# Performance work log

Hardware: AMD Instinct MI355X
Metric: run time of the kernel (lower is better)

The kernel has to match this reference:

```python
import jax, jax.numpy as jnp
import numpy as np

NUM_HEADS = 8
C = 512


def setup_inputs() -> dict:
    key = jax.random.key(0)
    ks = jax.random.split(key, 8)
    B, D, H, W = 1, 16, 16, 16
    x = jax.random.normal(ks[0], (B, C, D, H, W), dtype=jnp.float32)
    s = 1.0 / np.sqrt(C)
    Wq = jax.random.normal(ks[1], (C, C), dtype=jnp.float32) * s
    Wk = jax.random.normal(ks[2], (C, C), dtype=jnp.float32) * s
    Wv = jax.random.normal(ks[3], (C, C), dtype=jnp.float32) * s
    bq = jax.random.normal(ks[4], (C,), dtype=jnp.float32) * 0.01
    bk = jax.random.normal(ks[5], (C,), dtype=jnp.float32) * 0.01
    bv = jax.random.normal(ks[6], (C,), dtype=jnp.float32) * 0.01
    # torch inits gamma to 0; use 0.5 so the attention branch contributes
    gamma = jnp.full((1,), 0.5, dtype=jnp.float32)
    return {"x": x, "Wq": Wq, "bq": bq, "Wk": Wk, "bk": bk, "Wv": Wv, "bv": bv, "gamma": gamma}


def _attn(x, Wq, bq, Wk, bk, Wv, bv, gamma):
    B, Cc, D, H, W = x.shape
    nh = NUM_HEADS
    hd = Cc // nh
    N = D * H * W

    def proj(Wm, bm):
        # 1x1x1 Conv3d == channel GEMM
        y = jnp.einsum('oc,bcdhw->bodhw', Wm, x) + bm[None, :, None, None, None]
        y = y.reshape(B, nh, hd, D, H, W)            # [B, nh, hd, D, H, W]
        y = jnp.moveaxis(y, 2, -1)                    # [B, nh, D, H, W, hd]
        return y.reshape(B * nh, N, hd)               # [B*nh, N, hd]

    q = proj(Wq, bq)
    k = proj(Wk, bk)
    v = proj(Wv, bv)

    # NOTE: original module has NO 1/sqrt(head_dim) scaling -- faithful.
    energy = jnp.einsum('bnd,bmd->bnm', q, k)         # [B*nh, N, N]
    attention = jax.nn.softmax(energy, axis=-1)
    out = jnp.einsum('bnm,bmd->bnd', attention, v)    # [B*nh, N, hd]

    # Faithful (buggy-in-original) reshape: [B, N, nh, hd] row-major into [B, C, D, H, W]
    out = out.reshape(B, nh, N, hd).transpose(0, 2, 1, 3).reshape(B, Cc, D, H, W)
    return gamma[0] * out + x


def reference(x, Wq, bq, Wk, bk, Wv, bv, gamma):
    return _attn(x, Wq, bq, Wk, bk, Wv, bv, gamma)
```

## Files before the change

kernel.cpp:

```cpp
#include <hip/hip_runtime.h>

typedef unsigned short u16;
typedef __attribute__((ext_vector_type(4))) float f32x4;
typedef __attribute__((ext_vector_type(8))) short s16x8;
typedef __attribute__((ext_vector_type(4))) unsigned short u16x4;
typedef __attribute__((ext_vector_type(8))) unsigned short u16x8;
typedef __attribute__((ext_vector_type(2))) unsigned int u32x2;

#define MFMA(a, b, c) __builtin_amdgcn_mfma_f32_16x16x32_bf16((a), (b), (c), 0, 0, 0)

#define XT_HI 0u
#define XT_LO 2097152u
#define W_HI  4194304u
#define W_LO  4980736u
#define Q_HI  5767168u
#define Q_LO  7864320u
#define K_HI  9961472u
#define K_LO  12058624u
#define V_HI  14155776u
#define V_LO  16252928u
#define WS_BYTES_U16 36700160u

__device__ __forceinline__ u16 f2bf(float f) {
  union { float f; unsigned u; } v; v.f = f;
  unsigned r = v.u + 0x7fffu + ((v.u >> 16) & 1u);
  return (u16)(r >> 16);
}
__device__ __forceinline__ float bf2f(u16 h) {
  union { unsigned u; float f; } v; v.u = ((unsigned)h) << 16;
  return v.f;
}
__device__ __forceinline__ unsigned pk2(float a, float b) {
  return (unsigned)f2bf(a) | ((unsigned)f2bf(b) << 16);
}
__device__ __forceinline__ void gload16(const void* g, void* l) {
  __builtin_amdgcn_global_load_lds(
      (const __attribute__((address_space(1))) void*)g,
      (__attribute__((address_space(3))) void*)l, 16, 0, 0);
}

__global__ __launch_bounds__(256) void prep_w(const float* __restrict__ wq,
                                              const float* __restrict__ wk,
                                              const float* __restrict__ wv,
                                              u16* __restrict__ ws) {
  unsigned t = blockIdx.x * 256u + threadIdx.x;
  unsigned idx = t * 4u;
  unsigned which = idx >> 18;
  unsigned rem = idx & 262143u;
  const float* src = (which == 0) ? wq : (which == 1) ? wk : wv;
  f32x4 v = *(const f32x4*)(src + rem);
  u16x4 h, l;
#pragma unroll
  for (int i = 0; i < 4; ++i) {
    u16 hb = f2bf(v[i]);
    h[i] = hb;
    l[i] = f2bf(v[i] - bf2f(hb));
  }
  *(u16x4*)(ws + W_HI + idx) = h;
  *(u16x4*)(ws + W_LO + idx) = l;
}

__global__ __launch_bounds__(256) void prep_xt(const float* __restrict__ x,
                                               u16* __restrict__ ws) {
  __shared__ float tile[64][65];
  unsigned t = threadIdx.x;
  unsigned n0 = blockIdx.x * 64u, c0 = blockIdx.y * 64u;
  unsigned cl = t >> 2, ns = (t & 3u) * 16u;
  const float* src = x + (c0 + cl) * 4096u + n0 + ns;
#pragma unroll
  for (int j = 0; j < 16; j += 4) {
    f32x4 v = *(const f32x4*)(src + j);
#pragma unroll
    for (int e = 0; e < 4; ++e) tile[cl][ns + j + e] = v[e];
  }
  __syncthreads();
  unsigned nl = t >> 2, cs = (t & 3u) * 16u;
  u16x8 vh0, vh1, vl0, vl1;
#pragma unroll
  for (int j = 0; j < 16; ++j) {
    float v = tile[cs + j][nl];
    u16 hb = f2bf(v);
    u16 lb = f2bf(v - bf2f(hb));
    if (j < 8) { vh0[j] = hb; vl0[j] = lb; }
    else       { vh1[j - 8] = hb; vl1[j - 8] = lb; }
  }
  unsigned off = (n0 + nl) * 512u + c0 + cs;
  *(u16x8*)(ws + XT_HI + off) = vh0;
  *(u16x8*)(ws + XT_HI + off + 8u) = vh1;
  *(u16x8*)(ws + XT_LO + off) = vl0;
  *(u16x8*)(ws + XT_LO + off + 8u) = vl1;
}

__global__ __launch_bounds__(256) void proj(const float* __restrict__ bq,
                                            const float* __restrict__ bk,
                                            const float* __restrict__ bv,
                                            u16* __restrict__ ws) {
  __shared__ u16 sm[24576];
  const unsigned t = threadIdx.x, w = t >> 6, lane = t & 63u;
  const unsigned g4 = lane >> 4, c = lane & 15u;
  const unsigned z = blockIdx.z;
  const unsigned m0 = blockIdx.y * 64u, n0 = blockIdx.x * 128u;
  const unsigned wo = w >> 1, wn = w & 1u;

  const u16* WHp = ws + W_HI + z * 262144u;
  const u16* WLp = ws + W_LO + z * 262144u;
  const u16* XH = ws + XT_HI;
  const u16* XL = ws + XT_LO;

  f32x4 acc[2][4];
#pragma unroll
  for (int a = 0; a < 2; ++a)
#pragma unroll
    for (int b = 0; b < 4; ++b) acc[a][b] = (f32x4){0.f, 0.f, 0.f, 0.f};

  const unsigned r_l = lane >> 3;
  const unsigned cl_ = lane & 7u;

  for (unsigned it = 0; it < 8; ++it) {
    unsigned k0 = it * 64u;
#pragma unroll
    for (unsigned j = 0; j < 12; ++j) {
      unsigned s = w * 12u + j;
      if (s < 8u) {
        unsigned r = 8u * s + r_l; unsigned cg = cl_ ^ (r & 7u);
        gload16(WHp + (m0 + r) * 512u + k0 + 8u * cg, sm + s * 512u);
      } else if (s < 16u) {
        unsigned sl = s - 8u; unsigned r = 8u * sl + r_l; unsigned cg = cl_ ^ (r & 7u);
        gload16(WLp + (m0 + r) * 512u + k0 + 8u * cg, sm + 4096u + sl * 512u);
      } else if (s < 32u) {
        unsigned sl = s - 16u; unsigned r = 8u * sl + r_l; unsigned cg = cl_ ^ (r & 7u);
        gload16(XH + (n0 + r) * 512u + k0 + 8u * cg, sm + 8192u + sl * 512u);
      } else {
        unsigned sl = s - 32u; unsigned r = 8u * sl + r_l; unsigned cg = cl_ ^ (r & 7u);
        gload16(XL + (n0 + r) * 512u + k0 + 8u * cg, sm + 16384u + sl * 512u);
      }
    }
    __syncthreads();

    s16x8 ah[2][2], al[2][2];
#pragma unroll
    for (int mr = 0; mr < 2; ++mr)
#pragma unroll
      for (int ks = 0; ks < 2; ++ks) {
        unsigned row = 32u * wo + 16u * mr + c;
        unsigned idx = row * 64u + (((g4 + 4u * ks) ^ (row & 7u)) * 8u);
        ah[mr][ks] = *(const s16x8*)(sm + idx);
        al[mr][ks] = *(const s16x8*)(sm + 4096u + idx);
      }
#pragma unroll
    for (int ks = 0; ks < 2; ++ks)
#pragma unroll
      for (int nr = 0; nr < 4; ++nr) {
        unsigned row = 64u * wn + 16u * nr + c;
        unsigned idx = row * 64u + (((g4 + 4u * ks) ^ (row & 7u)) * 8u);
        s16x8 bh = *(const s16x8*)(sm + 8192u + idx);
        s16x8 bl = *(const s16x8*)(sm + 16384u + idx);
#pragma unroll
        for (int mr = 0; mr < 2; ++mr) {
          acc[mr][nr] = MFMA(ah[mr][ks], bh, acc[mr][nr]);
          acc[mr][nr] = MFMA(ah[mr][ks], bl, acc[mr][nr]);
          acc[mr][nr] = MFMA(al[mr][ks], bh, acc[mr][nr]);
        }
      }
    __syncthreads();
  }

  const float* bias = (z == 0) ? bq : (z == 1) ? bk : bv;
  const unsigned obase = m0 + 32u * wo;
#pragma unroll
  for (int mr = 0; mr < 2; ++mr) {
    f32x4 b4 = *(const f32x4*)(bias + obase + 16u * mr + 4u * g4);
#pragma unroll
    for (int nr = 0; nr < 4; ++nr) {
      unsigned n = n0 + 64u * wn + 16u * nr + c;
      float v4[4];
#pragma unroll
      for (int i = 0; i < 4; ++i) v4[i] = acc[mr][nr][i] + b4[i];
      if (z == 0u) {
        unsigned d0 = 32u * wo + 16u * mr + 4u * g4;
        unsigned off = (blockIdx.y * 4096u + n) * 64u + d0;
        u16x4 h4, l4;
#pragma unroll
        for (int i = 0; i < 4; ++i) {
          u16 hb = f2bf(v4[i]);
          h4[i] = hb;
          l4[i] = f2bf(v4[i] - bf2f(hb));
        }
        *(u16x4*)(ws + Q_HI + off) = h4;
        *(u16x4*)(ws + Q_LO + off) = l4;
      } else if (z == 1u) {
        unsigned d0 = 32u * wo + 16u * mr + 4u * g4;
        unsigned off = (blockIdx.y * 4096u + n) * 64u + d0;
        u16x4 h4;
#pragma unroll
        for (int i = 0; i < 4; ++i) h4[i] = f2bf(v4[i]);
        *(u16x4*)(ws + K_HI + off) = h4;
      } else {
#pragma unroll
        for (int i = 0; i < 4; ++i) {
          unsigned o = obase + 16u * mr + 4u * g4 + i;
          ws[V_HI + o * 4096u + n] = f2bf(v4[i]);
        }
      }
    }
  }
}

__global__ __launch_bounds__(256) void attn(const u16* __restrict__ ws,
                                            float* __restrict__ ows,
                                            float* __restrict__ lws) {
  extern __shared__ u16 sm[];
  const unsigned t = threadIdx.x, w = t >> 6, lane = t & 63u;
  const unsigned g4 = lane >> 4, c = lane & 15u;
  const unsigned h = blockIdx.y, sp = blockIdx.z;
  const unsigned q0 = blockIdx.x * 64u;

  const u16* QHp = ws + Q_HI; const u16* QLp = ws + Q_LO;
  const u16* KHp = ws + K_HI;
  const u16* VHp = ws + V_HI;

  s16x8 qh[2], ql[2];
#pragma unroll
  for (int ks = 0; ks < 2; ++ks) {
    unsigned q = q0 + 16u * w + c;
    unsigned off = (h * 4096u + q) * 64u + 8u * g4 + 32u * ks;
    qh[ks] = *(const s16x8*)(QHp + off);
    ql[ks] = *(const s16x8*)(QLp + off);
  }

  f32x4 O[4];
#pragma unroll
  for (int b = 0; b < 4; ++b) O[b] = (f32x4){0.f, 0.f, 0.f, 0.f};
  float lr = 0.f;

  const unsigned r_l = lane >> 3, cl_ = lane & 7u;
  u16* Pw = sm + 16384u + w * 1024u;

  auto stage = [&](unsigned b, unsigned ch) {
    unsigned n0 = sp * 2048u + ch * 64u;
#pragma unroll
    for (unsigned j = 0; j < 4u; ++j) {
      unsigned s = w * 4u + j;
      unsigned pl = s >> 3, sl = s & 7u;
      unsigned r = 8u * sl + r_l;
      unsigned cg = cl_ ^ (r & 7u);
      const u16* gsrc;
      if (pl == 0u) gsrc = KHp + (h * 4096u + n0 + r) * 64u + 8u * cg;
      else          gsrc = VHp + (h * 64u + r) * 4096u + n0 + 8u * cg;
      gload16(gsrc, sm + b * 8192u + pl * 4096u + sl * 512u);
    }
  };

  stage(0u, 0u);
  __syncthreads();

  unsigned cur = 0u;
  for (unsigned ch = 0; ch < 32u; ++ch) {
    if (ch < 31u) stage(cur ^ 1u, ch + 1u);
    const unsigned kb = cur * 8192u;

    f32x4 S[4];
#pragma unroll
    for (int b = 0; b < 4; ++b) S[b] = (f32x4){0.f, 0.f, 0.f, 0.f};
#pragma unroll
    for (int ks = 0; ks < 2; ++ks)
#pragma unroll
      for (int nr = 0; nr < 4; ++nr) {
        unsigned row = 16u * nr + c;
        unsigned idx = kb + row * 64u + (((g4 + 4u * ks) ^ (row & 7u)) * 8u);
        s16x8 kh = *(const s16x8*)(sm + idx);
        S[nr] = MFMA(kh, qh[ks], S[nr]);
        S[nr] = MFMA(kh, ql[ks], S[nr]);
      }

    {
      float ls = 0.f;
#pragma unroll
      for (int nr = 0; nr < 4; ++nr) {
        f32x4 s = S[nr];
        float p0 = __expf(s[0] - 40.0f);
        float p1 = __expf(s[1] - 40.0f);
        float p2 = __expf(s[2] - 40.0f);
        float p3 = __expf(s[3] - 40.0f);
        ls += (p0 + p1) + (p2 + p3);
        u32x2 pv;
        pv[0] = pk2(p0, p1);
        pv[1] = pk2(p2, p3);
        unsigned off = c * 64u + (((2u * nr + (g4 >> 1)) ^ (c & 7u)) * 8u) + (g4 & 1u) * 4u;
        *(u32x2*)(Pw + off) = pv;
      }
      ls += __shfl_xor(ls, 16);
      ls += __shfl_xor(ls, 32);
      lr += ls;
    }

#pragma unroll
    for (int ks = 0; ks < 2; ++ks) {
      s16x8 pa = *(const s16x8*)(Pw + c * 64u + (((g4 + 4u * ks) ^ (c & 7u)) * 8u));
#pragma unroll
      for (int nr = 0; nr < 4; ++nr) {
        unsigned row = 16u * nr + c;
        unsigned idx = kb + 4096u + row * 64u + (((g4 + 4u * ks) ^ (row & 7u)) * 8u);
        s16x8 vh = *(const s16x8*)(sm + idx);
        O[nr] = MFMA(pa, vh, O[nr]);
      }
    }
    __syncthreads();
    cur ^= 1u;
  }

#pragma unroll
  for (int i = 0; i < 4; ++i) {
    unsigned n = q0 + 16u * w + 4u * g4 + i;
    unsigned lwi = (sp * 8u + h) * 4096u + n;
#pragma unroll
    for (int nr = 0; nr < 4; ++nr)
      ows[lwi * 64u + 16u * nr + c] = O[nr][i];
  }
  if (lane < 16u)
    lws[(sp * 8u + h) * 4096u + q0 + 16u * w + lane] = lr;
}

__global__ __launch_bounds__(256) void combine(const float* __restrict__ x,
                                               const float* __restrict__ gamma,
                                               const float* __restrict__ ows,
                                               const float* __restrict__ lws,
                                               float* __restrict__ out) {
  unsigned t = blockIdx.x * 256u + threadIdx.x;
  unsigned L = t * 4u;
  unsigned n = L >> 9, hd6 = L & 511u, h = hd6 >> 6, d = L & 63u;
  unsigned i0 = (h * 4096u + n) * 64u + d;
  unsigned i1 = ((8u + h) * 4096u + n) * 64u + d;
  f32x4 a = *(const f32x4*)(ows + i0);
  f32x4 b = *(const f32x4*)(ows + i1);
  float l = lws[h * 4096u + n] + lws[(8u + h) * 4096u + n];
  float gi = gamma[0] / l;
  f32x4 xv = *(const f32x4*)(x + L);
  f32x4 r = (a + b) * gi + xv;
  *(f32x4*)(out + L) = r;
}

extern "C" void kernel_launch(void* const* d_in, const int* in_sizes, int n_in,
                              void* d_out, int out_size, void* d_ws, size_t ws_size,
                              hipStream_t stream) {
  const float* x = (const float*)d_in[0];
  const float* wq = (const float*)d_in[1];
  const float* bq = (const float*)d_in[2];
  const float* wk = (const float*)d_in[3];
  const float* bk = (const float*)d_in[4];
  const float* wv = (const float*)d_in[5];
  const float* bv = (const float*)d_in[6];
  const float* gamma = (const float*)d_in[7];
  u16* ws = (u16*)d_ws;
  float* ows = (float*)((char*)d_ws + WS_BYTES_U16);
  float* lws = ows + 4194304u;
  float* out = (float*)d_out;

  prep_w<<<dim3(768), dim3(256), 0, stream>>>(wq, wk, wv, ws);
  prep_xt<<<dim3(64, 8), dim3(256), 0, stream>>>(x, ws);
  proj<<<dim3(32, 8, 3), dim3(256), 0, stream>>>(bq, bk, bv, ws);
  (void)hipFuncSetAttribute((const void*)attn,
                            hipFuncAttributeMaxDynamicSharedMemorySize, 40960);
  attn<<<dim3(64, 8, 2), dim3(256), 40960, stream>>>(ws, ows, lws);
  combine<<<dim3(2048), dim3(256), 0, stream>>>(x, gamma, ows, lws, out);
}
```

Baseline: 188.1 us.

## Double-buffer projection GEMM, drop weight low-part, and streamline attention loop

```diff
diff --git a/kernel.cpp b/kernel.cpp
--- a/kernel.cpp
+++ b/kernel.cpp
@@ -30,8 +30,9 @@
   union { unsigned u; float f; } v; v.u = ((unsigned)h) << 16;
   return v.f;
 }
-__device__ __forceinline__ unsigned pk2(float a, float b) {
-  return (unsigned)f2bf(a) | ((unsigned)f2bf(b) << 16);
+__device__ __forceinline__ unsigned pk2h(float a, float b) {
+  union { float f; unsigned u; } ua, ub; ua.f = a; ub.f = b;
+  return __builtin_amdgcn_perm(ub.u + 0x8000u, ua.u + 0x8000u, 0x07060302u);
 }
 __device__ __forceinline__ void gload16(const void* g, void* l) {
   __builtin_amdgcn_global_load_lds(
@@ -49,15 +50,10 @@
   unsigned rem = idx & 262143u;
   const float* src = (which == 0) ? wq : (which == 1) ? wk : wv;
   f32x4 v = *(const f32x4*)(src + rem);
-  u16x4 h, l;
-#pragma unroll
-  for (int i = 0; i < 4; ++i) {
-    u16 hb = f2bf(v[i]);
-    h[i] = hb;
-    l[i] = f2bf(v[i] - bf2f(hb));
-  }
+  u16x4 h;
+#pragma unroll
+  for (int i = 0; i < 4; ++i) h[i] = f2bf(v[i]);
   *(u16x4*)(ws + W_HI + idx) = h;
-  *(u16x4*)(ws + W_LO + idx) = l;
 }
 
 __global__ __launch_bounds__(256) void prep_xt(const float* __restrict__ x,
@@ -95,7 +91,7 @@
                                             const float* __restrict__ bk,
                                             const float* __restrict__ bv,
                                             u16* __restrict__ ws) {
-  __shared__ u16 sm[24576];
+  extern __shared__ u16 sm[];
   const unsigned t = threadIdx.x, w = t >> 6, lane = t & 63u;
   const unsigned g4 = lane >> 4, c = lane & 15u;
   const unsigned z = blockIdx.z;
@@ -103,7 +99,6 @@
   const unsigned wo = w >> 1, wn = w & 1u;
 
   const u16* WHp = ws + W_HI + z * 262144u;
-  const u16* WLp = ws + W_LO + z * 262144u;
   const u16* XH = ws + XT_HI;
   const u16* XL = ws + XT_LO;
 
@@ -113,55 +108,55 @@
 #pragma unroll
     for (int b = 0; b < 4; ++b) acc[a][b] = (f32x4){0.f, 0.f, 0.f, 0.f};
 
-  const unsigned r_l = lane >> 3;
-  const unsigned cl_ = lane & 7u;
-
-  for (unsigned it = 0; it < 8; ++it) {
-    unsigned k0 = it * 64u;
-#pragma unroll
-    for (unsigned j = 0; j < 12; ++j) {
-      unsigned s = w * 12u + j;
-      if (s < 8u) {
-        unsigned r = 8u * s + r_l; unsigned cg = cl_ ^ (r & 7u);
-        gload16(WHp + (m0 + r) * 512u + k0 + 8u * cg, sm + s * 512u);
-      } else if (s < 16u) {
-        unsigned sl = s - 8u; unsigned r = 8u * sl + r_l; unsigned cg = cl_ ^ (r & 7u);
-        gload16(WLp + (m0 + r) * 512u + k0 + 8u * cg, sm + 4096u + sl * 512u);
-      } else if (s < 32u) {
-        unsigned sl = s - 16u; unsigned r = 8u * sl + r_l; unsigned cg = cl_ ^ (r & 7u);
-        gload16(XH + (n0 + r) * 512u + k0 + 8u * cg, sm + 8192u + sl * 512u);
-      } else {
-        unsigned sl = s - 32u; unsigned r = 8u * sl + r_l; unsigned cg = cl_ ^ (r & 7u);
-        gload16(XL + (n0 + r) * 512u + k0 + 8u * cg, sm + 16384u + sl * 512u);
+  const unsigned r_l = lane >> 2;
+  const unsigned cl_ = lane & 3u;
+
+  auto stage = [&](unsigned b, unsigned it) {
+    unsigned k0 = it * 32u;
+#pragma unroll
+    for (unsigned j = 0; j < 5u; ++j) {
+      unsigned s = w * 5u + j;
+      unsigned sl, dbase, rowoff; const u16* base;
+      if (s < 4u)       { sl = s;       dbase = 0u;    base = WHp; rowoff = m0; }
+      else if (s < 12u) { sl = s - 4u;  dbase = 2048u; base = XH;  rowoff = n0; }
+      else              { sl = s - 12u; dbase = 6144u; base = XL;  rowoff = n0; }
+      unsigned r = 16u * sl + r_l;
+      unsigned cg = cl_ ^ ((r >> 1) & 3u);
+      gload16(base + (rowoff + r) * 512u + k0 + 8u * cg,
+              sm + b * 10240u + dbase + sl * 512u);
+    }
+  };
+
+  auto body = [&](unsigned kb) {
+    s16x8 ah[2];
+#pragma unroll
+    for (int mr = 0; mr < 2; ++mr) {
+      unsigned row = 32u * wo + 16u * mr + c;
+      unsigned idx = kb + row * 32u + ((g4 ^ ((row >> 1) & 3u)) * 8u);
+      ah[mr] = *(const s16x8*)(sm + idx);
+    }
+#pragma unroll
+    for (int nr = 0; nr < 4; ++nr) {
+      unsigned row = 64u * wn + 16u * nr + c;
+      unsigned idx = kb + 2048u + row * 32u + ((g4 ^ ((row >> 1) & 3u)) * 8u);
+      s16x8 bh = *(const s16x8*)(sm + idx);
+      s16x8 bl = *(const s16x8*)(sm + idx + 4096u);
+#pragma unroll
+      for (int mr = 0; mr < 2; ++mr) {
+        acc[mr][nr] = MFMA(ah[mr], bh, acc[mr][nr]);
+        acc[mr][nr] = MFMA(ah[mr], bl, acc[mr][nr]);
       }
     }
+  };
+
+  stage(0u, 0u);
+  __syncthreads();
+  for (unsigned it = 0; it < 8u; ++it) {
+    stage(1u, 2u * it + 1u);
+    body(0u);
     __syncthreads();
-
-    s16x8 ah[2][2], al[2][2];
-#pragma unroll
-    for (int mr = 0; mr < 2; ++mr)
-#pragma unroll
-      for (int ks = 0; ks < 2; ++ks) {
-        unsigned row = 32u * wo + 16u * mr + c;
-        unsigned idx = row * 64u + (((g4 + 4u * ks) ^ (row & 7u)) * 8u);
-        ah[mr][ks] = *(const s16x8*)(sm + idx);
-        al[mr][ks] = *(const s16x8*)(sm + 4096u + idx);
-      }
-#pragma unroll
-    for (int ks = 0; ks < 2; ++ks)
-#pragma unroll
-      for (int nr = 0; nr < 4; ++nr) {
-        unsigned row = 64u * wn + 16u * nr + c;
-        unsigned idx = row * 64u + (((g4 + 4u * ks) ^ (row & 7u)) * 8u);
-        s16x8 bh = *(const s16x8*)(sm + 8192u + idx);
-        s16x8 bl = *(const s16x8*)(sm + 16384u + idx);
-#pragma unroll
-        for (int mr = 0; mr < 2; ++mr) {
-          acc[mr][nr] = MFMA(ah[mr][ks], bh, acc[mr][nr]);
-          acc[mr][nr] = MFMA(ah[mr][ks], bl, acc[mr][nr]);
-          acc[mr][nr] = MFMA(al[mr][ks], bh, acc[mr][nr]);
-        }
-      }
+    if (it < 7u) stage(0u, 2u * it + 2u);
+    body(10240u);
     __syncthreads();
   }
 
@@ -236,6 +231,20 @@
   const unsigned r_l = lane >> 3, cl_ = lane & 7u;
   u16* Pw = sm + 16384u + w * 1024u;
 
+  unsigned kidx[2][4], poff[4], paoff[2];
+#pragma unroll
+  for (int ks = 0; ks < 2; ++ks) {
+#pragma unroll
+    for (int nr = 0; nr < 4; ++nr) {
+      unsigned row = 16u * nr + c;
+      kidx[ks][nr] = row * 64u + (((g4 + 4u * ks) ^ (row & 7u)) * 8u);
+    }
+    paoff[ks] = c * 64u + (((g4 + 4u * ks) ^ (c & 7u)) * 8u);
+  }
+#pragma unroll
+  for (int nr = 0; nr < 4; ++nr)
+    poff[nr] = c * 64u + (((2u * nr + (g4 >> 1)) ^ (c & 7u)) * 8u) + (g4 & 1u) * 4u;
+
   auto stage = [&](unsigned b, unsigned ch) {
     unsigned n0 = sp * 2048u + ch * 64u;
 #pragma unroll
@@ -251,14 +260,7 @@
     }
   };
 
-  stage(0u, 0u);
-  __syncthreads();
-
-  unsigned cur = 0u;
-  for (unsigned ch = 0; ch < 32u; ++ch) {
-    if (ch < 31u) stage(cur ^ 1u, ch + 1u);
-    const unsigned kb = cur * 8192u;
-
+  auto body = [&](unsigned kb) {
     f32x4 S[4];
 #pragma unroll
     for (int b = 0; b < 4; ++b) S[b] = (f32x4){0.f, 0.f, 0.f, 0.f};
@@ -266,47 +268,47 @@
     for (int ks = 0; ks < 2; ++ks)
 #pragma unroll
       for (int nr = 0; nr < 4; ++nr) {
-        unsigned row = 16u * nr + c;
-        unsigned idx = kb + row * 64u + (((g4 + 4u * ks) ^ (row & 7u)) * 8u);
-        s16x8 kh = *(const s16x8*)(sm + idx);
+        s16x8 kh = *(const s16x8*)(sm + kb + kidx[ks][nr]);
         S[nr] = MFMA(kh, qh[ks], S[nr]);
         S[nr] = MFMA(kh, ql[ks], S[nr]);
       }
-
-    {
-      float ls = 0.f;
+    float ls = 0.f;
+#pragma unroll
+    for (int nr = 0; nr < 4; ++nr) {
+      f32x4 s = S[nr];
+      float p0 = __expf(s[0] - 40.0f);
+      float p1 = __expf(s[1] - 40.0f);
+      float p2 = __expf(s[2] - 40.0f);
+      float p3 = __expf(s[3] - 40.0f);
+      ls += (p0 + p1) + (p2 + p3);
+      u32x2 pv;
+      pv[0] = pk2h(p0, p1);
+      pv[1] = pk2h(p2, p3);
+      *(u32x2*)(Pw + poff[nr]) = pv;
+    }
+    ls += __shfl_xor(ls, 16);
+    ls += __shfl_xor(ls, 32);
+    lr += ls;
+#pragma unroll
+    for (int ks = 0; ks < 2; ++ks) {
+      s16x8 pa = *(const s16x8*)(Pw + paoff[ks]);
 #pragma unroll
       for (int nr = 0; nr < 4; ++nr) {
-        f32x4 s = S[nr];
-        float p0 = __expf(s[0] - 40.0f);
-        float p1 = __expf(s[1] - 40.0f);
-        float p2 = __expf(s[2] - 40.0f);
-        float p3 = __expf(s[3] - 40.0f);
-        ls += (p0 + p1) + (p2 + p3);
-        u32x2 pv;
-        pv[0] = pk2(p0, p1);
-        pv[1] = pk2(p2, p3);
-        unsigned off = c * 64u + (((2u * nr + (g4 >> 1)) ^ (c & 7u)) * 8u) + (g4 & 1u) * 4u;
-        *(u32x2*)(Pw + off) = pv;
-      }
-      ls += __shfl_xor(ls, 16);
-      ls += __shfl_xor(ls, 32);
-      lr += ls;
-    }
-
-#pragma unroll
-    for (int ks = 0; ks < 2; ++ks) {
-      s16x8 pa = *(const s16x8*)(Pw + c * 64u + (((g4 + 4u * ks) ^ (c & 7u)) * 8u));
-#pragma unroll
-      for (int nr = 0; nr < 4; ++nr) {
-        unsigned row = 16u * nr + c;
-        unsigned idx = kb + 4096u + row * 64u + (((g4 + 4u * ks) ^ (row & 7u)) * 8u);
-        s16x8 vh = *(const s16x8*)(sm + idx);
+        s16x8 vh = *(const s16x8*)(sm + kb + 4096u + kidx[ks][nr]);
         O[nr] = MFMA(pa, vh, O[nr]);
       }
     }
+  };
+
+  stage(0u, 0u);
+  __syncthreads();
+  for (unsigned it = 0; it < 16u; ++it) {
+    stage(1u, 2u * it + 1u);
+    body(0u);
     __syncthreads();
-    cur ^= 1u;
+    if (it < 15u) stage(0u, 2u * it + 2u);
+    body(8192u);
+    __syncthreads();
   }
 
 #pragma unroll
@@ -358,7 +360,9 @@
 
   prep_w<<<dim3(768), dim3(256), 0, stream>>>(wq, wk, wv, ws);
   prep_xt<<<dim3(64, 8), dim3(256), 0, stream>>>(x, ws);
-  proj<<<dim3(32, 8, 3), dim3(256), 0, stream>>>(bq, bk, bv, ws);
+  (void)hipFuncSetAttribute((const void*)proj,
+                            hipFuncAttributeMaxDynamicSharedMemorySize, 40960);
+  proj<<<dim3(32, 8, 3), dim3(256), 40960, stream>>>(bq, bk, bv, ws);
   (void)hipFuncSetAttribute((const void*)attn,
                             hipFuncAttributeMaxDynamicSharedMemorySize, 40960);
   attn<<<dim3(64, 8, 2), dim3(256), 40960, stream>>>(ws, ows, lws);
```

Result: faster. 174.2 us (-7.4%).
